# Kernel optimization log

Hardware: AMD Instinct MI355X
Metric: run time of the kernel (lower is better)

Reference implementation:

```python
import jax, jax.numpy as jnp
import numpy as np

MASK_DENSITY = 0.1  # fraction of nonzero weights kept by the sparsity mask


def setup_inputs() -> dict:
    key = jax.random.key(0)
    k_data, k_w, k_m, k_b = jax.random.split(key, 4)
    tokens, in_f, out_f = 8192, 4096, 4096
    data = jax.random.normal(k_data, (tokens, in_f), dtype=jnp.float32)
    weight = jax.random.normal(k_w, (out_f, in_f), dtype=jnp.float32)
    mask = (jax.random.uniform(k_m, (out_f, in_f)) < MASK_DENSITY).astype(jnp.float32)
    bias = jax.random.normal(k_b, (out_f,), dtype=jnp.float32)
    return {"data": data, "weight": weight, "mask": mask, "bias": bias}


def reference(data, weight, mask, bias):
    # out = data @ (mask * weight)^T + bias  (sparse linear; CSR of mask*weight
    # in the original kernel -- dense math is identical).
    w_sp = mask * weight                      # [out_f, in_f]
    out = jnp.einsum("ti,oi->to", data, w_sp) # [tokens, out_f]
    return out + bias
```

## Files before the change

### kernel.cpp

```cpp
#include <hip/hip_runtime.h>
#include <hip/hip_bf16.h>


#define GM 8192
#define GN 4096
#define GK 4096
#define NT (GK / 32)

typedef __attribute__((ext_vector_type(8))) short short8;
typedef __attribute__((ext_vector_type(8))) short bf16x8;
typedef __attribute__((ext_vector_type(4))) float f32x4;

__device__ __forceinline__ short f2bf(float x) {
    unsigned u = __builtin_bit_cast(unsigned, x);
    u += 0x7fffu + ((u >> 16) & 1u);
    return (short)(u >> 16);
}

__device__ __forceinline__ void stage16(const short* g, short* l) {
    __builtin_amdgcn_global_load_lds(
        (const __attribute__((address_space(1))) unsigned int*)g,
        (__attribute__((address_space(3))) unsigned int*)l, 16, 0, 0);
}

__global__ void cvt_data_kernel(const float* __restrict__ in, short* __restrict__ out, long n) {
    long i0 = ((long)blockIdx.x * blockDim.x + threadIdx.x) * 8;
    long stride = (long)gridDim.x * blockDim.x * 8;
    for (long i = i0; i < n; i += stride) {
        float4 a = *(const float4*)(in + i);
        float4 b = *(const float4*)(in + i + 4);
        short8 o;
        o[0] = f2bf(a.x); o[1] = f2bf(a.y); o[2] = f2bf(a.z); o[3] = f2bf(a.w);
        o[4] = f2bf(b.x); o[5] = f2bf(b.y); o[6] = f2bf(b.z); o[7] = f2bf(b.w);
        *(short8*)(out + i) = o;
    }
}

__global__ void cvt_w_kernel(const float* __restrict__ w, const float* __restrict__ m,
                             short* __restrict__ out, long n) {
    long i0 = ((long)blockIdx.x * blockDim.x + threadIdx.x) * 8;
    long stride = (long)gridDim.x * blockDim.x * 8;
    for (long i = i0; i < n; i += stride) {
        float4 wa = *(const float4*)(w + i);
        float4 wb = *(const float4*)(w + i + 4);
        float4 ma = *(const float4*)(m + i);
        float4 mb = *(const float4*)(m + i + 4);
        short8 o;
        o[0] = f2bf(wa.x * ma.x); o[1] = f2bf(wa.y * ma.y);
        o[2] = f2bf(wa.z * ma.z); o[3] = f2bf(wa.w * ma.w);
        o[4] = f2bf(wb.x * mb.x); o[5] = f2bf(wb.y * mb.y);
        o[6] = f2bf(wb.z * mb.z); o[7] = f2bf(wb.w * mb.w);
        *(short8*)(out + i) = o;
    }
}

__global__ __launch_bounds__(512, 2) void gemm_8w(const short* __restrict__ A,
                                                  const short* __restrict__ B,
                                                  const float* __restrict__ bias,
                                                  float* __restrict__ C) {
    __shared__ short lds[65536];

    const int tid  = threadIdx.x;
    const int lane = tid & 63;
    const int wid  = tid >> 6;
    const int wr   = wid >> 2;
    const int wc   = wid & 3;

    const int bid  = blockIdx.x;
    const int swz  = (bid & 7) * 64 + (bid >> 3);
    const int brow = (swz >> 4) << 8;
    const int bcol = (swz & 15) << 8;

    const int lrow  = tid >> 2;
    const int q_log = (tid & 3) ^ ((((lrow >> 3) & 1) << 1) | ((lrow >> 1) & 1));
    const size_t aSrc0 = (size_t)(brow + lrow) * GK + q_log * 8;
    const size_t bSrc0 = (size_t)(bcol + lrow) * GK + q_log * 8;

    const int l15 = lane & 15;
    const int q   = lane >> 4;
    const int qx  = (((l15 >> 3) & 1) << 1) | ((l15 >> 1) & 1);
    const int foff = l15 * 32 + ((q ^ qx) << 3);
    const int aOff = wr * 4096 + foff;
    const int bOff = 8192 + (wc >> 1) * 4096 + (wc & 1) * 2048 + foff;

    f32x4 acc[8][4] = {};
    bf16x8 afA[4], afB[4], bfA[4], bfB[4];

    auto stageA = [&](int t) {
        const int ring = (t & 3) * 16384;
        const size_t k = (size_t)t * 32;
        #pragma unroll
        for (int h = 0; h < 2; ++h)
            stage16(A + aSrc0 + (size_t)h * 128 * GK + k, &lds[ring + h * 4096 + wid * 512]);
    };
    auto stageB = [&](int t) {
        const int ring = (t & 3) * 16384;
        const size_t k = (size_t)t * 32;
        #pragma unroll
        for (int h = 0; h < 2; ++h)
            stage16(B + bSrc0 + (size_t)h * 128 * GK + k, &lds[ring + 8192 + h * 4096 + wid * 512]);
    };

    stageA(0); stageB(0);
    stageA(1); stageB(1);
    stageA(2); stageB(2);
    asm volatile("s_waitcnt vmcnt(4)" ::: "memory");
    __builtin_amdgcn_s_barrier();
    asm volatile("" ::: "memory");
    #pragma unroll
    for (int m = 0; m < 4; ++m) afA[m] = *(const bf16x8*)&lds[aOff + m * 512];
    #pragma unroll
    for (int n = 0; n < 4; ++n) bfA[n] = *(const bf16x8*)&lds[bOff + n * 512];

#define TILE_BODY(T, AF_P0, AF_P1, BF_CUR, BF_NXT)                                 \
  {                                                                                 \
    const int ring  = ((T) & 3) * 16384;                                            \
    const int ringN = (((T) + 1) & 3) * 16384;                                      \
                                                             \
    if ((T) + 3 < NT) stageA((T) + 3);                                              \
    _Pragma("unroll")                                                               \
    for (int m = 0; m < 4; ++m)                                                     \
      AF_P1[m] = *(const bf16x8*)&lds[ring + aOff + (m + 4) * 512];                 \
    __builtin_amdgcn_sched_barrier(0);                                              \
    __builtin_amdgcn_s_setprio(1);                                                  \
    _Pragma("unroll")                                                               \
    for (int m = 0; m < 4; ++m)                                                     \
      _Pragma("unroll")                                                             \
      for (int n = 0; n < 4; ++n)                                                   \
        acc[m][n] = __builtin_amdgcn_mfma_f32_16x16x32_bf16(AF_P0[m], BF_CUR[n],    \
                                                            acc[m][n], 0, 0, 0);    \
    __builtin_amdgcn_s_setprio(0);                                                  \
       \
    if ((T) + 3 < NT) stageB((T) + 3);                                              \
    _Pragma("unroll")                                                               \
    for (int m = 0; m < 4; ++m)                                                     \
      AF_P0[m] = *(const bf16x8*)&lds[ringN + aOff + m * 512];                      \
    _Pragma("unroll")                                                               \
    for (int n = 0; n < 4; ++n)                                                     \
      BF_NXT[n] = *(const bf16x8*)&lds[ringN + bOff + n * 512];                     \
    __builtin_amdgcn_sched_barrier(0);                                              \
    __builtin_amdgcn_s_setprio(1);                                                  \
    _Pragma("unroll")                                                               \
    for (int m = 0; m < 4; ++m)                                                     \
      _Pragma("unroll")                                                             \
      for (int n = 0; n < 4; ++n)                                                   \
        acc[m + 4][n] = __builtin_amdgcn_mfma_f32_16x16x32_bf16(AF_P1[m], BF_CUR[n],\
                                                                acc[m + 4][n], 0, 0, 0); \
    __builtin_amdgcn_s_setprio(0);                                                  \
    if ((T) + 3 < NT) { asm volatile("s_waitcnt vmcnt(4)" ::: "memory"); }          \
    else              { asm volatile("s_waitcnt vmcnt(0)" ::: "memory"); }          \
    __builtin_amdgcn_s_barrier();                                                   \
    asm volatile("" ::: "memory");                                                  \
  }

    for (int T = 0; T < NT; T += 2) {
        TILE_BODY(T,     afA, afB, bfA, bfB);
        TILE_BODY(T + 1, afA, afB, bfB, bfA);
    }
#undef TILE_BODY

    #pragma unroll
    for (int n = 0; n < 4; ++n) {
        const int col = bcol + wc * 64 + n * 16 + l15;
        const float bv = bias[col];
        #pragma unroll
        for (int m = 0; m < 8; ++m) {
            const int rowb = brow + wr * 128 + m * 16 + (q << 2);
            #pragma unroll
            for (int r = 0; r < 4; ++r)
                C[(size_t)(rowb + r) * GN + col] = acc[m][n][r] + bv;
        }
    }
}

extern "C" void kernel_launch(void* const* d_in, const int* in_sizes, int n_in,
                              void* d_out, int out_size, void* d_ws, size_t ws_size,
                              hipStream_t stream) {
    const float* data   = (const float*)d_in[0];
    const float* weight = (const float*)d_in[1];
    const float* mask   = (const float*)d_in[2];
    const float* bias   = (const float*)d_in[3];
    float* out = (float*)d_out;

    short* dataB = (short*)d_ws;
    short* wB    = dataB + (size_t)GM * GK;

    cvt_data_kernel<<<2048, 256, 0, stream>>>(data, dataB, (long)GM * GK);
    cvt_w_kernel<<<2048, 256, 0, stream>>>(weight, mask, wB, (long)GN * GK);

    gemm_8w<<<512, 512, 0, stream>>>(dataB, wB, bias, out);
}
```

Before: 296.7 us.

## Switch GEMM inner loop from 16x16x32 to 32x32x16 bf16 MFMA

Replaces the 16x16x32 MFMA tiling with 32x32x16 MFMA instructions, reorganizing the per-wave fragments into 4x2 tiles of 32x32 with two K sub-steps per 32-wide K slice. The LDS swizzle and fragment addressing are changed to match the new operand layout, and the epilogue store mapping is updated for the 16-register accumulator layout. The aim is fewer MFMA issues and fewer LDS fragment reads per unit of work, at the cost of a different bank-conflict pattern and a more scattered output store.

```diff
diff --git a/kernel.cpp b/kernel.cpp
--- a/kernel.cpp
+++ b/kernel.cpp
@@ -9,7 +9,7 @@
 
 typedef __attribute__((ext_vector_type(8))) short short8;
 typedef __attribute__((ext_vector_type(8))) short bf16x8;
-typedef __attribute__((ext_vector_type(4))) float f32x4;
+typedef __attribute__((ext_vector_type(16))) float f32x16;
 
 __device__ __forceinline__ short f2bf(float x) {
     unsigned u = __builtin_bit_cast(unsigned, x);
@@ -72,19 +72,21 @@
     const int bcol = (swz & 15) << 8;
 
     const int lrow  = tid >> 2;
-    const int q_log = (tid & 3) ^ ((((lrow >> 3) & 1) << 1) | ((lrow >> 1) & 1));
+    const int q_log = (tid & 3) ^ (((lrow >> 1) & 1) | (((lrow >> 2) & 1) << 1));
     const size_t aSrc0 = (size_t)(brow + lrow) * GK + q_log * 8;
     const size_t bSrc0 = (size_t)(bcol + lrow) * GK + q_log * 8;
 
-    const int l15 = lane & 15;
-    const int q   = lane >> 4;
-    const int qx  = (((l15 >> 3) & 1) << 1) | ((l15 >> 1) & 1);
-    const int foff = l15 * 32 + ((q ^ qx) << 3);
-    const int aOff = wr * 4096 + foff;
-    const int bOff = 8192 + (wc >> 1) * 4096 + (wc & 1) * 2048 + foff;
-
-    f32x4 acc[8][4] = {};
-    bf16x8 afA[4], afB[4], bfA[4], bfB[4];
+    const int l31 = lane & 31;
+    const int l5  = lane >> 5;
+    const int qxl = ((lane >> 1) & 1) | (((lane >> 2) & 1) << 1);
+    const int q0  = l5 ^ qxl;
+    const int aK0 = l31 * 32 + q0 * 8;
+    const int aK1 = l31 * 32 + (q0 ^ 2) * 8;
+    const int aBase = wr * 4096;
+    const int bBase = 8192 + (wc >> 1) * 4096 + (wc & 1) * 2048;
+
+    f32x16 acc[4][2] = {};
+    bf16x8 AF_P0[4], AF_P1[4], BF_A[4], BF_B[4];
 
     auto stageA = [&](int t) {
         const int ring = (t & 3) * 16384;
@@ -108,44 +110,60 @@
     __builtin_amdgcn_s_barrier();
     asm volatile("" ::: "memory");
     #pragma unroll
-    for (int m = 0; m < 4; ++m) afA[m] = *(const bf16x8*)&lds[aOff + m * 512];
+    for (int m = 0; m < 2; ++m) {
+        AF_P0[m * 2 + 0] = *(const bf16x8*)&lds[aBase + m * 1024 + aK0];
+        AF_P0[m * 2 + 1] = *(const bf16x8*)&lds[aBase + m * 1024 + aK1];
+    }
     #pragma unroll
-    for (int n = 0; n < 4; ++n) bfA[n] = *(const bf16x8*)&lds[bOff + n * 512];
-
-#define TILE_BODY(T, AF_P0, AF_P1, BF_CUR, BF_NXT)                                 \
+    for (int n = 0; n < 2; ++n) {
+        BF_A[n * 2 + 0] = *(const bf16x8*)&lds[bBase + n * 1024 + aK0];
+        BF_A[n * 2 + 1] = *(const bf16x8*)&lds[bBase + n * 1024 + aK1];
+    }
+
+#define TILE_BODY(T, BF_CUR, BF_NXT)                                               \
   {                                                                                 \
     const int ring  = ((T) & 3) * 16384;                                            \
     const int ringN = (((T) + 1) & 3) * 16384;                                      \
-                                                             \
+                        \
     if ((T) + 3 < NT) stageA((T) + 3);                                              \
     _Pragma("unroll")                                                               \
-    for (int m = 0; m < 4; ++m)                                                     \
-      AF_P1[m] = *(const bf16x8*)&lds[ring + aOff + (m + 4) * 512];                 \
+    for (int m = 0; m < 2; ++m) {                                                   \
+      AF_P1[m * 2 + 0] = *(const bf16x8*)&lds[ring + aBase + (m + 2) * 1024 + aK0]; \
+      AF_P1[m * 2 + 1] = *(const bf16x8*)&lds[ring + aBase + (m + 2) * 1024 + aK1]; \
+    }                                                                               \
     __builtin_amdgcn_sched_barrier(0);                                              \
     __builtin_amdgcn_s_setprio(1);                                                  \
     _Pragma("unroll")                                                               \
-    for (int m = 0; m < 4; ++m)                                                     \
+    for (int m = 0; m < 2; ++m)                                                     \
       _Pragma("unroll")                                                             \
-      for (int n = 0; n < 4; ++n)                                                   \
-        acc[m][n] = __builtin_amdgcn_mfma_f32_16x16x32_bf16(AF_P0[m], BF_CUR[n],    \
-                                                            acc[m][n], 0, 0, 0);    \
+      for (int n = 0; n < 2; ++n)                                                   \
+        _Pragma("unroll")                                                           \
+        for (int ks = 0; ks < 2; ++ks)                                              \
+          acc[m][n] = __builtin_amdgcn_mfma_f32_32x32x16_bf16(                      \
+              AF_P0[m * 2 + ks], BF_CUR[n * 2 + ks], acc[m][n], 0, 0, 0);           \
     __builtin_amdgcn_s_setprio(0);                                                  \
-       \
+                  \
     if ((T) + 3 < NT) stageB((T) + 3);                                              \
     _Pragma("unroll")                                                               \
-    for (int m = 0; m < 4; ++m)                                                     \
-      AF_P0[m] = *(const bf16x8*)&lds[ringN + aOff + m * 512];                      \
-    _Pragma("unroll")                                                               \
-    for (int n = 0; n < 4; ++n)                                                     \
-      BF_NXT[n] = *(const bf16x8*)&lds[ringN + bOff + n * 512];                     \
+    for (int m = 0; m < 2; ++m) {                                                   \
+      AF_P0[m * 2 + 0] = *(const bf16x8*)&lds[ringN + aBase + m * 1024 + aK0];      \
+      AF_P0[m * 2 + 1] = *(const bf16x8*)&lds[ringN + aBase + m * 1024 + aK1];      \
+    }                                                                               \
+    _Pragma("unroll")                                                               \
+    for (int n = 0; n < 2; ++n) {                                                   \
+      BF_NXT[n * 2 + 0] = *(const bf16x8*)&lds[ringN + bBase + n * 1024 + aK0];     \
+      BF_NXT[n * 2 + 1] = *(const bf16x8*)&lds[ringN + bBase + n * 1024 + aK1];     \
+    }                                                                               \
     __builtin_amdgcn_sched_barrier(0);                                              \
     __builtin_amdgcn_s_setprio(1);                                                  \
     _Pragma("unroll")                                                               \
-    for (int m = 0; m < 4; ++m)                                                     \
+    for (int m = 0; m < 2; ++m)                                                     \
       _Pragma("unroll")                                                             \
-      for (int n = 0; n < 4; ++n)                                                   \
-        acc[m + 4][n] = __builtin_amdgcn_mfma_f32_16x16x32_bf16(AF_P1[m], BF_CUR[n],\
-                                                                acc[m + 4][n], 0, 0, 0); \
+      for (int n = 0; n < 2; ++n)                                                   \
+        _Pragma("unroll")                                                           \
+        for (int ks = 0; ks < 2; ++ks)                                              \
+          acc[m + 2][n] = __builtin_amdgcn_mfma_f32_32x32x16_bf16(                  \
+              AF_P1[m * 2 + ks], BF_CUR[n * 2 + ks], acc[m + 2][n], 0, 0, 0);       \
     __builtin_amdgcn_s_setprio(0);                                                  \
     if ((T) + 3 < NT) { asm volatile("s_waitcnt vmcnt(4)" ::: "memory"); }          \
     else              { asm volatile("s_waitcnt vmcnt(0)" ::: "memory"); }          \
@@ -154,21 +172,23 @@
   }
 
     for (int T = 0; T < NT; T += 2) {
-        TILE_BODY(T,     afA, afB, bfA, bfB);
-        TILE_BODY(T + 1, afA, afB, bfB, bfA);
+        TILE_BODY(T,     BF_A, BF_B);
+        TILE_BODY(T + 1, BF_B, BF_A);
     }
 #undef TILE_BODY
 
     #pragma unroll
-    for (int n = 0; n < 4; ++n) {
-        const int col = bcol + wc * 64 + n * 16 + l15;
+    for (int n = 0; n < 2; ++n) {
+        const int col = bcol + wc * 64 + n * 32 + l31;
         const float bv = bias[col];
         #pragma unroll
-        for (int m = 0; m < 8; ++m) {
-            const int rowb = brow + wr * 128 + m * 16 + (q << 2);
+        for (int m = 0; m < 4; ++m) {
+            const int rowb = brow + wr * 128 + m * 32 + l5 * 4;
             #pragma unroll
-            for (int r = 0; r < 4; ++r)
-                C[(size_t)(rowb + r) * GN + col] = acc[m][n][r] + bv;
+            for (int reg = 0; reg < 16; ++reg) {
+                const int row = rowb + (reg & 3) + 8 * (reg >> 2);
+                C[(size_t)row * GN + col] = acc[m][n][reg] + bv;
+            }
         }
     }
 }
```

Result: slower. 303.8 us (+2.4%).
